# Kernel optimization log

Measured on AMD Instinct MI355X. Metric: run time of the kernel, lower is better.

Reference implementation:

```python
import jax, jax.numpy as jnp
import numpy as np

NUM_ENT = 50000
NUM_REL = 500
DIM = 128
BATCH = 32
INIT_RHO = -5.0


def setup_inputs() -> dict:
    key = jax.random.key(0)
    k1, k2, k3 = jax.random.split(key, 3)
    ent_center = jax.random.uniform(k1, (NUM_ENT, 2 * DIM), minval=-0.1, maxval=0.1, dtype=jnp.float32)
    ent_rho = jnp.full((NUM_ENT, DIM), INIT_RHO, dtype=jnp.float32)
    rel_center = jax.random.uniform(k2, (NUM_REL, DIM), minval=-np.pi, maxval=np.pi, dtype=jnp.float32)
    rel_rho = jnp.full((NUM_REL, DIM), INIT_RHO, dtype=jnp.float32)
    pos_triplets = jax.random.randint(k3, (BATCH, 3), 0, NUM_REL, dtype=jnp.int64)
    return {
        "ent_center": ent_center,
        "ent_rho": ent_rho,
        "rel_center": rel_center,
        "rel_rho": rel_rho,
        "pos_triplets": pos_triplets,
    }


def reference(ent_center, ent_rho, rel_center, rel_rho, pos_triplets):
    # All-entity embeddings: center split into (re, im) halves, radius via softplus.
    u_re, u_im = jnp.split(ent_center, 2, axis=-1)          # [N, D] each
    u_r = jax.nn.softplus(ent_rho)                           # [N, D]

    h_idx = pos_triplets[:, 0]
    r_idx = pos_triplets[:, 1]

    hc = ent_center[h_idx]                                   # [B, 2D]
    hr = jax.nn.softplus(ent_rho[h_idx])                     # [B, D]
    rc_phase = rel_center[r_idx]                             # [B, D]
    rr = jax.nn.softplus(rel_rho[r_idx])                     # [B, D]

    hc_re, hc_im = jnp.split(hc, 2, axis=-1)                 # [B, D]
    cos_r = jnp.cos(rc_phase)
    sin_r = jnp.sin(rc_phase)
    pred_re = hc_re * cos_r - hc_im * sin_r                  # [B, D]
    pred_im = hc_re * sin_r + hc_im * cos_r                  # [B, D]
    pred_r = hr + rr                                         # [B, D]

    # Broadcast L2 (complex magnitude) distance to every entity: [B, N]
    diff_re = pred_re[:, None, :] - u_re[None, :, :]         # [B, N, D]
    diff_im = pred_im[:, None, :] - u_im[None, :, :]         # [B, N, D]
    dist_c = jnp.sqrt(diff_re ** 2 + diff_im ** 2).sum(axis=-1)  # [B, N]

    # sum over dim of (pred_r + u_r) broadcast == sum(pred_r) + sum(u_r)
    sum_r = pred_r.sum(axis=-1)[:, None] + u_r.sum(axis=-1)[None, :]  # [B, N]
    return sum_r - dist_c
```

## Files before the change

### kernel.cpp

```cpp
#include <hip/hip_runtime.h>
#include <math.h>

#define NENT 50000
#define NREL 500
#define DIMK 128
#define BATCH 32

#define WS_PRED 0
#define WS_PSUM 8192
#define WS_URSUM 8224

__device__ __forceinline__ float softplus_f(float x) {
    float e = __expf(-fabsf(x));
    return fmaxf(x, 0.0f) + __logf(1.0f + e);
}

__device__ __forceinline__ float fast_sqrtf(float x) {
#if __has_builtin(__builtin_amdgcn_sqrtf)
    return __builtin_amdgcn_sqrtf(x);
#else
    return sqrtf(x);
#endif
}

__device__ __forceinline__ float RL(float v, int l) {
    return __uint_as_float(__builtin_amdgcn_readlane(__float_as_uint(v), l));
}

__device__ __forceinline__ int get_idx(const void* trip, int flat) {
    const long long* t64 = (const long long*)trip;
    const int* t32 = (const int*)trip;
    bool is64 = true;
    #pragma unroll 1
    for (int i = 0; i < 48; ++i) {
        long long v = t64[i];
        if (v < 0 || v >= NREL) { is64 = false; break; }
    }
    return is64 ? (int)t64[flat] : t32[flat];
}

__global__ __launch_bounds__(128)
void prep_kernel(const float* __restrict__ ent_center,
                 const float* __restrict__ ent_rho,
                 const float* __restrict__ rel_center,
                 const float* __restrict__ rel_rho,
                 const void* __restrict__ trip,
                 float* __restrict__ ws) {
    const int b = blockIdx.x;
    const int d = threadIdx.x;
    const int h = get_idx(trip, b * 3 + 0);
    const int r = get_idx(trip, b * 3 + 1);

    float hre = ent_center[h * 256 + d];
    float him = ent_center[h * 256 + 128 + d];
    float ph  = rel_center[r * 128 + d];
    float s = sinf(ph), c = cosf(ph);
    ws[WS_PRED + (b * 128 + d) * 2 + 0] = hre * c - him * s;
    ws[WS_PRED + (b * 128 + d) * 2 + 1] = hre * s + him * c;

    float pr = softplus_f(ent_rho[h * 128 + d]) + softplus_f(rel_rho[r * 128 + d]);
    #pragma unroll
    for (int off = 32; off > 0; off >>= 1) pr += __shfl_down(pr, off);
    __shared__ float tmp[2];
    if ((threadIdx.x & 63) == 0) tmp[threadIdx.x >> 6] = pr;
    __syncthreads();
    if (threadIdx.x == 0) ws[WS_PSUM + b] = tmp[0] + tmp[1];
}

__global__ __launch_bounds__(256)
void ursum_kernel(const float* __restrict__ ent_rho, float* __restrict__ ws) {
    const int wave = threadIdx.x >> 6, lane = threadIdx.x & 63;
    const int e = blockIdx.x * 4 + wave;
    if (e >= NENT) return;
    float2 v = *(const float2*)(ent_rho + (size_t)e * 128 + lane * 2);
    float s = softplus_f(v.x) + softplus_f(v.y);
    #pragma unroll
    for (int off = 32; off > 0; off >>= 1) s += __shfl_down(s, off);
    if (lane == 0) ws[WS_URSUM + e] = s;
}

__global__ __launch_bounds__(256, 4)
void score_kernel(const float* __restrict__ ent_center,
                  const float* __restrict__ ws,
                  float* __restrict__ out) {
    __shared__ float4 s_stage[1024];

    const int tid = threadIdx.x;
    const int lane = tid & 63;
    const int wv = tid >> 6;
    const int e0 = blockIdx.x * 64;
    const int q = tid & 7;
    const int et = tid >> 3;
    const float4* cen4 = (const float4*)ent_center;

    const float* pbase = ws + WS_PRED + (size_t)(wv * 8 + (lane >> 3)) * 256 + (lane & 7);

    float4 g[4];
    auto GLOAD = [&](int c) {
        #pragma unroll
        for (int s = 0; s < 2; ++s)
            #pragma unroll
            for (int r = 0; r < 2; ++r) {
                int ge = e0 + (et & 31) + 32 * r;
                if (ge > NENT - 1) ge = NENT - 1;
                g[s * 2 + r] = cen4[(size_t)ge * 64 + s * 32 + c * 8 + q];
            }
    };
    auto DSWRITE = [&]() {
        #pragma unroll
        for (int s = 0; s < 2; ++s)
            #pragma unroll
            for (int r = 0; r < 2; ++r) {
                int ee = (et & 31) + 32 * r;
                s_stage[(s * 8 + q) * 64 + (ee ^ q)] = g[s * 2 + r];
            }
    };

    float acc[8];
    #pragma unroll
    for (int b = 0; b < 8; ++b) acc[b] = 0.0f;

    GLOAD(0);
    #pragma unroll 1
    for (int c = 0; c < 4; ++c) {
        if (c) __syncthreads();
        DSWRITE();
        if (c < 3) GLOAD(c + 1);
        float P[8];
        #pragma unroll
        for (int k = 0; k < 8; ++k) P[k] = pbase[c * 64 + k * 8];
        __syncthreads();

        #pragma unroll
        for (int dq = 0; dq < 8; ++dq) {
            const float4 ur = s_stage[dq * 64 + (lane ^ dq)];
            const float4 ui = s_stage[(8 + dq) * 64 + (lane ^ dq)];
            #pragma unroll
            for (int bb = 0; bb < 8; ++bb) {
                float dre, dmi, t;
                dre = RL(P[dq], bb * 8 + 0) - ur.x; dmi = RL(P[dq], bb * 8 + 1) - ui.x;
                t = dre * dre + dmi * dmi; acc[bb] += fast_sqrtf(t);
                dre = RL(P[dq], bb * 8 + 2) - ur.y; dmi = RL(P[dq], bb * 8 + 3) - ui.y;
                t = dre * dre + dmi * dmi; acc[bb] += fast_sqrtf(t);
                dre = RL(P[dq], bb * 8 + 4) - ur.z; dmi = RL(P[dq], bb * 8 + 5) - ui.z;
                t = dre * dre + dmi * dmi; acc[bb] += fast_sqrtf(t);
                dre = RL(P[dq], bb * 8 + 6) - ur.w; dmi = RL(P[dq], bb * 8 + 7) - ui.w;
                t = dre * dre + dmi * dmi; acc[bb] += fast_sqrtf(t);
            }
        }
    }

    const int e = e0 + lane;
    if (e < NENT) {
        const float ursum = ws[WS_URSUM + e];
        #pragma unroll
        for (int bb = 0; bb < 8; ++bb) {
            const int b = wv * 8 + bb;
            out[(size_t)b * NENT + e] = ws[WS_PSUM + b] + ursum - acc[bb];
        }
    }
}

extern "C" void kernel_launch(void* const* d_in, const int* in_sizes, int n_in,
                              void* d_out, int out_size, void* d_ws, size_t ws_size,
                              hipStream_t stream) {
    const float* ent_center = (const float*)d_in[0];
    const float* ent_rho    = (const float*)d_in[1];
    const float* rel_center = (const float*)d_in[2];
    const float* rel_rho    = (const float*)d_in[3];
    const void*  trip       = d_in[4];
    float* ws  = (float*)d_ws;
    float* out = (float*)d_out;

    ursum_kernel<<<(NENT + 3) / 4, 256, 0, stream>>>(ent_rho, ws);
    prep_kernel<<<BATCH, 128, 0, stream>>>(ent_center, ent_rho, rel_center, rel_rho, trip, ws);
    score_kernel<<<(NENT + 63) / 64, 256, 0, stream>>>(ent_center, ws, out);
}
```

Before: 169.4 us.

## Split batch across two grid rows and preload prediction lanes in registers

The score kernel now launches a second grid dimension that splits the 32 batch rows into two halves of 16. Each wave handles 4 batch rows instead of 8, and every prediction value is loaded into registers once up front rather than per chunk. The chunk loop is fully unrolled with a scheduling barrier after the prefetch, and the occupancy hint is raised to 8 blocks per CU. This doubles the block count and cuts per-thread register use, at the cost of each block re-reading the entity centers, which doubles global and LDS staging traffic for the same output.

```diff
diff --git a/kernel.cpp b/kernel.cpp
--- a/kernel.cpp
+++ b/kernel.cpp
@@ -79,7 +79,7 @@
     if (lane == 0) ws[WS_URSUM + e] = s;
 }
 
-__global__ __launch_bounds__(256, 4)
+__global__ __launch_bounds__(256, 8)
 void score_kernel(const float* __restrict__ ent_center,
                   const float* __restrict__ ws,
                   float* __restrict__ out) {
@@ -88,12 +88,20 @@
     const int tid = threadIdx.x;
     const int lane = tid & 63;
     const int wv = tid >> 6;
+    const int by = blockIdx.y;
     const int e0 = blockIdx.x * 64;
     const int q = tid & 7;
-    const int et = tid >> 3;
+    const int et = (tid >> 3) & 31;
     const float4* cen4 = (const float4*)ent_center;
 
-    const float* pbase = ws + WS_PRED + (size_t)(wv * 8 + (lane >> 3)) * 256 + (lane & 7);
+    const int pb = by * 16 + wv * 4 + ((lane >> 3) & 3);
+    const float* pbase = ws + WS_PRED + (size_t)pb * 256 + (lane & 7) + (lane >> 5) * 128;
+
+    float P[2][8];
+    #pragma unroll
+    for (int j = 0; j < 2; ++j)
+        #pragma unroll
+        for (int k = 0; k < 8; ++k) P[j][k] = pbase[j * 64 + k * 8];
 
     float4 g[4];
     auto GLOAD = [&](int c) {
@@ -101,7 +109,7 @@
         for (int s = 0; s < 2; ++s)
             #pragma unroll
             for (int r = 0; r < 2; ++r) {
-                int ge = e0 + (et & 31) + 32 * r;
+                int ge = e0 + et + 32 * r;
                 if (ge > NENT - 1) ge = NENT - 1;
                 g[s * 2 + r] = cen4[(size_t)ge * 64 + s * 32 + c * 8 + q];
             }
@@ -111,41 +119,41 @@
         for (int s = 0; s < 2; ++s)
             #pragma unroll
             for (int r = 0; r < 2; ++r) {
-                int ee = (et & 31) + 32 * r;
+                int ee = et + 32 * r;
                 s_stage[(s * 8 + q) * 64 + (ee ^ q)] = g[s * 2 + r];
             }
     };
 
-    float acc[8];
-    #pragma unroll
-    for (int b = 0; b < 8; ++b) acc[b] = 0.0f;
+    float acc[4] = {0.0f, 0.0f, 0.0f, 0.0f};
 
     GLOAD(0);
-    #pragma unroll 1
+    #pragma unroll
     for (int c = 0; c < 4; ++c) {
         if (c) __syncthreads();
         DSWRITE();
-        if (c < 3) GLOAD(c + 1);
-        float P[8];
-        #pragma unroll
-        for (int k = 0; k < 8; ++k) P[k] = pbase[c * 64 + k * 8];
         __syncthreads();
-
+        if (c < 3) {
+            GLOAD(c + 1);
+            __builtin_amdgcn_sched_barrier(0);
+        }
+        const int hi = (c >> 1) * 32;
         #pragma unroll
         for (int dq = 0; dq < 8; ++dq) {
             const float4 ur = s_stage[dq * 64 + (lane ^ dq)];
             const float4 ui = s_stage[(8 + dq) * 64 + (lane ^ dq)];
+            const float p = P[c & 1][dq];
             #pragma unroll
-            for (int bb = 0; bb < 8; ++bb) {
+            for (int bb = 0; bb < 4; ++bb) {
+                const int L = bb * 8 + hi;
                 float dre, dmi, t;
-                dre = RL(P[dq], bb * 8 + 0) - ur.x; dmi = RL(P[dq], bb * 8 + 1) - ui.x;
-                t = dre * dre + dmi * dmi; acc[bb] += fast_sqrtf(t);
-                dre = RL(P[dq], bb * 8 + 2) - ur.y; dmi = RL(P[dq], bb * 8 + 3) - ui.y;
-                t = dre * dre + dmi * dmi; acc[bb] += fast_sqrtf(t);
-                dre = RL(P[dq], bb * 8 + 4) - ur.z; dmi = RL(P[dq], bb * 8 + 5) - ui.z;
-                t = dre * dre + dmi * dmi; acc[bb] += fast_sqrtf(t);
-                dre = RL(P[dq], bb * 8 + 6) - ur.w; dmi = RL(P[dq], bb * 8 + 7) - ui.w;
-                t = dre * dre + dmi * dmi; acc[bb] += fast_sqrtf(t);
+                dre = RL(p, L + 0) - ur.x; dmi = RL(p, L + 1) - ui.x;
+                t = fmaf(dre, dre, dmi * dmi); acc[bb] += fast_sqrtf(t);
+                dre = RL(p, L + 2) - ur.y; dmi = RL(p, L + 3) - ui.y;
+                t = fmaf(dre, dre, dmi * dmi); acc[bb] += fast_sqrtf(t);
+                dre = RL(p, L + 4) - ur.z; dmi = RL(p, L + 5) - ui.z;
+                t = fmaf(dre, dre, dmi * dmi); acc[bb] += fast_sqrtf(t);
+                dre = RL(p, L + 6) - ur.w; dmi = RL(p, L + 7) - ui.w;
+                t = fmaf(dre, dre, dmi * dmi); acc[bb] += fast_sqrtf(t);
             }
         }
     }
@@ -154,8 +162,8 @@
     if (e < NENT) {
         const float ursum = ws[WS_URSUM + e];
         #pragma unroll
-        for (int bb = 0; bb < 8; ++bb) {
-            const int b = wv * 8 + bb;
+        for (int bb = 0; bb < 4; ++bb) {
+            const int b = by * 16 + wv * 4 + bb;
             out[(size_t)b * NENT + e] = ws[WS_PSUM + b] + ursum - acc[bb];
         }
     }
@@ -174,5 +182,6 @@
 
     ursum_kernel<<<(NENT + 3) / 4, 256, 0, stream>>>(ent_rho, ws);
     prep_kernel<<<BATCH, 128, 0, stream>>>(ent_center, ent_rho, rel_center, rel_rho, trip, ws);
-    score_kernel<<<(NENT + 63) / 64, 256, 0, stream>>>(ent_center, ws, out);
+    dim3 grid((NENT + 63) / 64, 2);
+    score_kernel<<<grid, 256, 0, stream>>>(ent_center, ws, out);
 }
```

New measurement: 492.3 us. 2.91x slower.
